# Kernel optimization log

Hardware: AMD Instinct MI355X
Metric: run time of the kernel (lower is better)

The kernel has to match this reference:

```python
import jax, jax.numpy as jnp
import numpy as np
from jax import lax

B, C, CI, H, W_SP = 8, 64, 3, 224, 224  # batch, per-channel groups, in-chans per group, spatial
K, STRIDE = 5, 2


def setup_inputs() -> dict:
    key = jax.random.key(0)
    kx, kw = jax.random.split(key)
    x = jax.random.normal(kx, (B, C, CI, H, W_SP), dtype=jnp.float32)
    # one Conv2d(3->1, k=5, stride=2, bias=False) per output channel -> stacked [C, CI, K, K]
    fan_in = CI * K * K
    bound = 1.0 / np.sqrt(fan_in)
    W = jax.random.uniform(kw, (C, CI, K, K), dtype=jnp.float32, minval=-bound, maxval=bound)
    return {"x": x, "W": W}


def reference(x, W):
    # x: [B, C, CI, H, W]; each of the C groups has its own 3->1 conv (weights W[c]).
    # Equivalent to a single grouped conv: input [B, C*CI, H, W], feature_group_count=C.
    b, c, ci, h, w = x.shape
    x2 = x.reshape(b, c * ci, h, w)
    out = lax.conv_general_dilated(
        x2, W,
        window_strides=(STRIDE, STRIDE),
        padding="VALID",
        feature_group_count=c,
        dimension_numbers=("NCHW", "OIHW", "NCHW"),
    )  # [B, C, H_out, W_out]
    return out
```

## Files before the change

kernel.cpp:

```cpp
#include <hip/hip_runtime.h>

#define BATCH 8
#define CH 64
#define CIN 3
#define HIN 224
#define WIN 224
#define KSZ 5
#define STRIDE 2
#define HO 110
#define WO 110
#define RY 10
#define RX 2
#define GROUPS (HO / RY)
#define PAIRS (WO / RX)
#define ITEMS (GROUPS * PAIRS)
#define TPB 128
#define BLOCKS_X ((ITEMS + TPB - 1) / TPB)
#define NPLANES (BATCH * CH)
#define NWG (BLOCKS_X * NPLANES)
#define NROWS (STRIDE * (RY - 1) + KSZ)
#define RWIDTH (STRIDE * (RX - 1) + KSZ)

typedef float float4a __attribute__((ext_vector_type(4)));
typedef float float2a __attribute__((ext_vector_type(2)));

__global__ __launch_bounds__(TPB) void conv5_reg2_kernel(
    const float* __restrict__ x,
    const float* __restrict__ Wt,
    float* __restrict__ out)
{
    __shared__ float wsh[CIN * KSZ * KSZ];

    const int wg = blockIdx.x;
    const int per = NWG >> 3;
    const int swz = (wg & 7) * per + (wg >> 3);
    const int bc   = swz / BLOCKS_X;
    const int xblk = swz - bc * BLOCKS_X;
    const int c = bc & (CH - 1);

    const int tid = threadIdx.x;
    if (tid < CIN * KSZ * KSZ) {
        wsh[tid] = Wt[c * (CIN * KSZ * KSZ) + tid];
    }
    __syncthreads();

    const int idx = xblk * TPB + tid;
    if (idx >= ITEMS) return;

    const int px = idx % PAIRS;
    const int g  = idx / PAIRS;
    const int ho0 = g * RY;
    const int ih0 = ho0 * STRIDE;
    const int iw0 = px * (RX * STRIDE);

    float acc[RY][RX];
#pragma unroll
    for (int t = 0; t < RY; ++t)
#pragma unroll
        for (int u = 0; u < RX; ++u) acc[t][u] = 0.f;

    const float* xb = x + (size_t)bc * (CIN * HIN * WIN);

#pragma unroll
    for (int ci = 0; ci < CIN; ++ci) {
        float wr[KSZ * KSZ];
#pragma unroll
        for (int i = 0; i < KSZ * KSZ; ++i) wr[i] = wsh[ci * KSZ * KSZ + i];

        const float* xp = xb + (size_t)ci * HIN * WIN + (size_t)ih0 * WIN + iw0;
#pragma unroll
        for (int r = 0; r < NROWS; ++r) {
            const float* rp = xp + r * WIN;
            float4a v0 = *reinterpret_cast<const float4a*>(rp);
            float4a v1 = *reinterpret_cast<const float4a*>(rp + 4);
            float xv[8] = {v0.x, v0.y, v0.z, v0.w, v1.x, v1.y, v1.z, v1.w};
#pragma unroll
            for (int t = 0; t < RY; ++t) {
                const int kh = r - STRIDE * t;
                if (kh >= 0 && kh < KSZ) {
#pragma unroll
                    for (int kw = 0; kw < KSZ; ++kw) {
                        const float w = wr[kh * KSZ + kw];
                        acc[t][0] = fmaf(xv[kw],     w, acc[t][0]);
                        acc[t][1] = fmaf(xv[kw + 2], w, acc[t][1]);
                    }
                }
            }
        }
    }

    float* op = out + (size_t)bc * (HO * WO) + (size_t)ho0 * WO + px * RX;
#pragma unroll
    for (int t = 0; t < RY; ++t) {
        float2a v = {acc[t][0], acc[t][1]};
        *reinterpret_cast<float2a*>(op + (size_t)t * WO) = v;
    }
}

extern "C" void kernel_launch(void* const* d_in, const int* in_sizes, int n_in,
                              void* d_out, int out_size, void* d_ws, size_t ws_size,
                              hipStream_t stream)
{
    const float* x  = (const float*)d_in[0];
    const float* Wt = (const float*)d_in[1];
    float* out = (float*)d_out;

    conv5_reg2_kernel<<<dim3(NWG), dim3(TPB), 0, stream>>>(x, Wt, out);
}
```

Measured before the change: 84.02 us.

## Stage input row slabs in LDS via direct global-to-LDS loads

Each workgroup now owns one 10-output-row tile of a plane. It copies the needed 23 input rows of all three channels into shared memory using global_load_lds 16-byte transfers, then computes 5x2 outputs per thread from LDS. This drops the overlapping global reads between neighbouring threads and rows that the old register-blocked kernel issued. In exchange it uses about 62KB of LDS per block, which limits occupancy, and only 110 of the 128 threads do compute.

```diff
diff --git a/kernel.cpp b/kernel.cpp
--- a/kernel.cpp
+++ b/kernel.cpp
@@ -9,57 +9,72 @@
 #define STRIDE 2
 #define HO 110
 #define WO 110
-#define RY 10
-#define RX 2
-#define GROUPS (HO / RY)
-#define PAIRS (WO / RX)
-#define ITEMS (GROUPS * PAIRS)
+
+#define TROWS 10
+#define TILES (HO / TROWS)
+#define NPLANES (BATCH * CH)
+#define NWG (NPLANES * TILES)
+#define INROWS (STRIDE * (TROWS - 1) + KSZ)
+#define SLABF (INROWS * WIN)
+#define SLABU (SLABF / 4)
+#define TOTU (CIN * SLABU)
 #define TPB 128
-#define BLOCKS_X ((ITEMS + TPB - 1) / TPB)
-#define NPLANES (BATCH * CH)
-#define NWG (BLOCKS_X * NPLANES)
-#define NROWS (STRIDE * (RY - 1) + KSZ)
-#define RWIDTH (STRIDE * (RX - 1) + KSZ)
+#define NITER ((TOTU + TPB - 1) / TPB)
 
 typedef float float4a __attribute__((ext_vector_type(4)));
 typedef float float2a __attribute__((ext_vector_type(2)));
 
-__global__ __launch_bounds__(TPB) void conv5_reg2_kernel(
+#define GLOAD_LDS16(gsrc, ldsdst) \
+    __builtin_amdgcn_global_load_lds((const __attribute__((address_space(1))) void*)(gsrc), \
+                                     (__attribute__((address_space(3))) void*)(ldsdst), 16, 0, 0)
+
+__global__ __launch_bounds__(TPB) void conv5_lds_kernel(
     const float* __restrict__ x,
     const float* __restrict__ Wt,
     float* __restrict__ out)
 {
+    __shared__ float xs[CIN * SLABF];
     __shared__ float wsh[CIN * KSZ * KSZ];
 
-    const int wg = blockIdx.x;
+    const int wg  = blockIdx.x;
     const int per = NWG >> 3;
     const int swz = (wg & 7) * per + (wg >> 3);
-    const int bc   = swz / BLOCKS_X;
-    const int xblk = swz - bc * BLOCKS_X;
+    const int bc   = swz / TILES;
+    const int tile = swz - bc * TILES;
     const int c = bc & (CH - 1);
+    const int ho0 = tile * TROWS;
+    const int ih0 = ho0 * STRIDE;
 
     const int tid = threadIdx.x;
     if (tid < CIN * KSZ * KSZ) {
         wsh[tid] = Wt[c * (CIN * KSZ * KSZ) + tid];
     }
+
+    const char* gbase = (const char*)(x + (size_t)bc * (CIN * HIN * WIN));
+#pragma unroll
+    for (int k = 0; k < NITER; ++k) {
+        const int u = k * TPB + tid;
+        const int ci = (u >= 2 * SLABU) ? 2 : (u >= SLABU ? 1 : 0);
+        const int rem = u - ci * SLABU;
+        const char* src = gbase + (size_t)ci * (HIN * WIN * 4)
+                                + (size_t)ih0 * (WIN * 4)
+                                + (size_t)rem * 16;
+        char* dst = (char*)xs + (size_t)(k * TPB + (tid & ~63)) * 16;
+        if (u < TOTU) {
+            GLOAD_LDS16(src, dst);
+        }
+    }
+
     __syncthreads();
 
-    const int idx = xblk * TPB + tid;
-    if (idx >= ITEMS) return;
+    if (tid >= 110) return;
+    const int px = tid % 55;
+    const int ty = tid / 55;
+    const int r0 = 10 * ty;
 
-    const int px = idx % PAIRS;
-    const int g  = idx / PAIRS;
-    const int ho0 = g * RY;
-    const int ih0 = ho0 * STRIDE;
-    const int iw0 = px * (RX * STRIDE);
-
-    float acc[RY][RX];
+    float acc[5][2];
 #pragma unroll
-    for (int t = 0; t < RY; ++t)
-#pragma unroll
-        for (int u = 0; u < RX; ++u) acc[t][u] = 0.f;
-
-    const float* xb = x + (size_t)bc * (CIN * HIN * WIN);
+    for (int t = 0; t < 5; ++t) { acc[t][0] = 0.f; acc[t][1] = 0.f; }
 
 #pragma unroll
     for (int ci = 0; ci < CIN; ++ci) {
@@ -67,16 +82,15 @@
 #pragma unroll
         for (int i = 0; i < KSZ * KSZ; ++i) wr[i] = wsh[ci * KSZ * KSZ + i];
 
-        const float* xp = xb + (size_t)ci * HIN * WIN + (size_t)ih0 * WIN + iw0;
+        const float* sp = xs + ci * SLABF + r0 * WIN + 4 * px;
 #pragma unroll
-        for (int r = 0; r < NROWS; ++r) {
-            const float* rp = xp + r * WIN;
-            float4a v0 = *reinterpret_cast<const float4a*>(rp);
-            float4a v1 = *reinterpret_cast<const float4a*>(rp + 4);
+        for (int rr = 0; rr < 13; ++rr) {
+            float4a v0 = *(const float4a*)(sp + rr * WIN);
+            float4a v1 = *(const float4a*)(sp + rr * WIN + 4);
             float xv[8] = {v0.x, v0.y, v0.z, v0.w, v1.x, v1.y, v1.z, v1.w};
 #pragma unroll
-            for (int t = 0; t < RY; ++t) {
-                const int kh = r - STRIDE * t;
+            for (int t = 0; t < 5; ++t) {
+                const int kh = rr - STRIDE * t;
                 if (kh >= 0 && kh < KSZ) {
 #pragma unroll
                     for (int kw = 0; kw < KSZ; ++kw) {
@@ -89,11 +103,11 @@
         }
     }
 
-    float* op = out + (size_t)bc * (HO * WO) + (size_t)ho0 * WO + px * RX;
+    float* op = out + (size_t)bc * (HO * WO) + (size_t)(ho0 + 5 * ty) * WO + 2 * px;
 #pragma unroll
-    for (int t = 0; t < RY; ++t) {
+    for (int t = 0; t < 5; ++t) {
         float2a v = {acc[t][0], acc[t][1]};
-        *reinterpret_cast<float2a*>(op + (size_t)t * WO) = v;
+        *(float2a*)(op + (size_t)t * WO) = v;
     }
 }
 
@@ -105,5 +119,5 @@
     const float* Wt = (const float*)d_in[1];
     float* out = (float*)d_out;
 
-    conv5_reg2_kernel<<<dim3(NWG), dim3(TPB), 0, stream>>>(x, Wt, out);
+    conv5_lds_kernel<<<dim3(NWG), dim3(TPB), 0, stream>>>(x, Wt, out);
 }
```

Result: faster. 74.24 us (-11.6%).
